# Performance work log

Hardware: AMD Instinct MI355X
Metric: run time of the kernel (lower is better)

Reference implementation:

```python
import jax, jax.numpy as jnp
import numpy as np

NEG = -1e30  # effective -inf that stays stable in fp32 log-sum-exp
BLANK = 0


def _lse3(a, b, c):
    m = jnp.maximum(jnp.maximum(a, b), c)
    return m + jnp.log(jnp.exp(a - m) + jnp.exp(b - m) + jnp.exp(c - m))


def _ctc_loss_sum(log_probs, input_lengths, targets, target_lengths):
    # log_probs: [B, T, V] already log-softmaxed; targets: [B, S] int, blank=0
    B, T, V = log_probs.shape
    S = targets.shape[1]
    L = 2 * S + 1  # extended label seq: blank-interleaved

    ext = jnp.full((B, L), BLANK, dtype=targets.dtype)
    ext = ext.at[:, 1::2].set(targets)  # [B, L]

    # gather per-frame log-probs of extended labels: [B, T, L]
    lp_ext = jnp.take_along_axis(
        log_probs, jnp.broadcast_to(ext[:, None, :], (B, T, L)), axis=2)

    # skip transition s-2 -> s allowed iff ext[s] != blank and ext[s] != ext[s-2]
    ext_prev2 = jnp.pad(ext[:, :-2], ((0, 0), (2, 0)), constant_values=BLANK)
    can_skip = (ext != BLANK) & (ext != ext_prev2) & (jnp.arange(L)[None, :] >= 2)

    # alpha init at t=0
    alpha = jnp.full((B, L), NEG, dtype=log_probs.dtype)
    alpha = alpha.at[:, 0].set(lp_ext[:, 0, 0])
    alpha = alpha.at[:, 1].set(lp_ext[:, 0, 1])

    lp_seq = jnp.swapaxes(lp_ext, 0, 1)[1:]          # [T-1, B, L]
    valid = jnp.arange(1, T)[:, None] < input_lengths[None, :]  # [T-1, B]

    def step(a, xs):
        lp_t, v = xs  # [B, L], [B]
        a1 = jnp.pad(a[:, :-1], ((0, 0), (1, 0)), constant_values=NEG)
        a2 = jnp.pad(a[:, :-2], ((0, 0), (2, 0)), constant_values=NEG)
        a2 = jnp.where(can_skip, a2, NEG)
        new = _lse3(a, a1, a2) + lp_t
        a = jnp.where(v[:, None], new, a)  # freeze past each utterance's length
        return a, None

    alpha, _ = jax.lax.scan(step, alpha, (lp_seq, valid))

    # terminal states: last blank (2*tl) and last label (2*tl - 1)
    end = 2 * target_lengths.astype(jnp.int32)
    aT = jnp.take_along_axis(alpha, jnp.stack([end, end - 1], axis=1), axis=1)  # [B, 2]
    ll = jax.scipy.special.logsumexp(aT, axis=1)
    loss = -ll
    loss = jnp.where(loss > 1e29, 0.0, loss)  # zero_infinity=True
    return jnp.sum(loss)  # reduction='sum'


def setup_inputs() -> dict:
    B, T, V, S = 64, 1024, 512, 128
    key = jax.random.key(0)
    k1, k2, k3, k4 = jax.random.split(key, 4)
    output_tensor = jax.random.normal(k1, (B, T, V), dtype=jnp.float32)
    output_lengths = jax.random.randint(k2, (B,), T // 2, T + 1, dtype=jnp.int32)
    target_tensor = jax.random.randint(k3, (B, S), 1, V, dtype=jnp.int32)  # no blanks
    target_lengths = jax.random.randint(k4, (B,), S // 2, S + 1, dtype=jnp.int32)
    return {"output_tensor": output_tensor, "output_lengths": output_lengths,
            "target_tensor": target_tensor, "target_lengths": target_lengths}


def reference(output_tensor, output_lengths, target_tensor, target_lengths):
    log_probs = jax.nn.log_softmax(output_tensor, axis=2)
    return _ctc_loss_sum(log_probs, output_lengths, target_tensor, target_lengths)
```

## Files before the change

kernel.cpp:

```cpp
#include <hip/hip_runtime.h>
#include <cstdint>

#define T_LEN 1024
#define V_DIM 512
#define S_LEN 128
#define NEG2  (-1.0e30f)
#define PREP_BLOCKS 2048
#define ROWS_PER_WAVE 8

__device__ float2 g_plab[(size_t)64 * T_LEN * 64 + 64];
__device__ float  g_pblank[(size_t)64 * T_LEN + 64];

static __device__ __forceinline__ float dpp_shr1_f(float x) {
    return __int_as_float(__builtin_amdgcn_update_dpp(
        0, __float_as_int(x), 0x138, 0xF, 0xF, true));
}
static __device__ __forceinline__ int dpp_shr1_i(int x) {
    return __builtin_amdgcn_update_dpp(0, x, 0x138, 0xF, 0xF, true);
}
template <int CTRL>
static __device__ __forceinline__ float dpp_add(float x) {
    const int y = __builtin_amdgcn_update_dpp(0, __float_as_int(x), CTRL, 0xF, 0xF, true);
    return x + __int_as_float(y);
}

__global__ __launch_bounds__(256) void ctc_prep(
    const float* __restrict__ x, const int* __restrict__ lens,
    const int* __restrict__ tgts)
{
    const int lane = threadIdx.x & 63;
    const int wv0  = (int)((blockIdx.x * blockDim.x + threadIdx.x) >> 6);
    const float L2E = 1.44269504088896340736f;

    #pragma unroll
    for (int it = 0; it < ROWS_PER_WAVE; ++it) {
        const int wid = wv0 + it * 8192;
        const int b = wid >> 10;
        const int t = wid & (T_LEN - 1);
        if (t >= lens[b]) continue;

        const float* row = x + (size_t)wid * V_DIM;
        const float4 u = *(const float4*)(row + lane * 8);
        const float4 v = *(const float4*)(row + lane * 8 + 4);

        float s = exp2f(u.x * L2E) + exp2f(u.y * L2E)
                + exp2f(u.z * L2E) + exp2f(u.w * L2E)
                + exp2f(v.x * L2E) + exp2f(v.y * L2E)
                + exp2f(v.z * L2E) + exp2f(v.w * L2E);
        s = dpp_add<0x111>(s);
        s = dpp_add<0x112>(s);
        s = dpp_add<0x114>(s);
        s = dpp_add<0x118>(s);
        s = dpp_add<0x142>(s);
        s = dpp_add<0x143>(s);
        const float off =
            log2f(__int_as_float(__builtin_amdgcn_readlane(__float_as_int(s), 63)));

        if (lane == 0) g_pblank[wid] = exp2f(u.x * L2E - off);

        const int2 tg = *(const int2*)(tgts + b * S_LEN + 2 * lane);
        g_plab[(size_t)wid * 64 + lane] =
            make_float2(exp2f(row[tg.x] * L2E - off), exp2f(row[tg.y] * L2E - off));
    }
}

struct AlphaState { float a0, a1, a2, a3, a4; int C; };

static __device__ __forceinline__ void alpha_step(
    AlphaState& st, float pb, float2 lp, float cs1f, float cs3f, bool dead)
{
    const float p3 = dpp_shr1_f(st.a3);
    const int   Cp = dpp_shr1_i(st.C);
    const int   Cn = dead ? Cp : st.C;
    int e = 127 + (Cp - Cn);
    e = e < 0 ? 0 : (e > 252 ? 252 : e);
    const float adj = __int_as_float((unsigned)e << 23);
    const float p3v = p3 * adj;
    const float s01 = st.a0 + st.a1;
    const float s23 = st.a2 + st.a3;
    const float n0 = (st.a0 + p3v) * pb;
    const float n1 = fmaf(p3v, cs1f, s01) * lp.x;
    const float n2 = (st.a1 + st.a2) * pb;
    const float n3 = fmaf(st.a1, cs3f, s23) * lp.y;
    const float n4 = (st.a3 + st.a4) * pb;
    st.a0 = n0; st.a1 = n1; st.a2 = n2; st.a3 = n3; st.a4 = n4; st.C = Cn;
}

static __device__ __forceinline__ void lean_step(
    AlphaState& st, float pb, float2 lp, float cs1f, float cs3f, float adj)
{
    const float p3 = dpp_shr1_f(st.a3);
    const float p3v = p3 * adj;
    const float s01 = st.a0 + st.a1;
    const float s23 = st.a2 + st.a3;
    const float n0 = (st.a0 + p3v) * pb;
    const float n1 = fmaf(p3v, cs1f, s01) * lp.x;
    const float n2 = (st.a1 + st.a2) * pb;
    const float n3 = fmaf(st.a1, cs3f, s23) * lp.y;
    const float n4 = (st.a3 + st.a4) * pb;
    st.a0 = n0; st.a1 = n1; st.a2 = n2; st.a3 = n3; st.a4 = n4;
}

static __device__ __forceinline__ void alpha_rescale(AlphaState& st)
{
    const float mx = fmaxf(fmaxf(fmaxf(st.a0, st.a1), fmaxf(st.a2, st.a3)), st.a4);
    const int ee = (__float_as_int(mx) >> 23) & 255;
    const bool ok = (ee > 0) && (ee < 255);
    const float sc = ok ? __int_as_float((unsigned)(254 - ee) << 23) : 1.0f;
    const int dC = ok ? (ee - 127) : 0;
    st.a0 *= sc; st.a1 *= sc; st.a2 *= sc; st.a3 *= sc; st.a4 *= sc; st.C += dC;
}

struct LGrp  { float2 v[16]; };
struct PBGrp { float4 a, b, c, d; };

static __device__ __forceinline__ float pbsel(const PBGrp& p, int i) {
    const float4 q = (i < 4) ? p.a : (i < 8) ? p.b : (i < 12) ? p.c : p.d;
    const int m = i & 3;
    return m == 0 ? q.x : m == 1 ? q.y : m == 2 ? q.z : q.w;
}

static __device__ __forceinline__ void issueL(
    LGrp& L, const float2* __restrict__ pl_b, int tb, int lenm1, int lane)
{
    #pragma unroll
    for (int j = 0; j < 16; ++j) {
        int r = tb + j; r = (r < lenm1) ? r : lenm1;
        L.v[j] = pl_b[(size_t)r * 64 + lane];
    }
}

static __device__ __forceinline__ void loadPB(PBGrp& P, const float* s) {
    P.a = *(const float4*)(s);
    P.b = *(const float4*)(s + 4);
    P.c = *(const float4*)(s + 8);
    P.d = *(const float4*)(s + 12);
}

template<bool LEAN>
static __device__ __forceinline__ void computeG16(
    AlphaState& st, const LGrp& L, const PBGrp& P,
    float cs1f, float cs3f, int tb, int deadline)
{
    float adj = 1.0f;
    #pragma unroll
    for (int i = 0; i < 16; ++i) {
        if (LEAN) {
            if ((i & 3) == 0) {
                const int Cp = dpp_shr1_i(st.C);
                int e = 127 + (Cp - st.C);
                e = e < 0 ? 0 : (e > 252 ? 252 : e);
                adj = __int_as_float((unsigned)e << 23);
            }
            lean_step(st, pbsel(P, i), L.v[i], cs1f, cs3f, adj);
        } else {
            alpha_step(st, pbsel(P, i), L.v[i], cs1f, cs3f, deadline >= tb + i);
        }
        if ((i & 3) == 3) alpha_rescale(st);
    }
}

static __device__ __forceinline__ void tail_steps(
    AlphaState& st, const LGrp& L, const PBGrp& P,
    float cs1f, float cs3f, int t0, int len, int deadline)
{
    #pragma unroll
    for (int i = 0; i < 15; ++i) {
        if (t0 + i < len) {
            alpha_step(st, pbsel(P, i), L.v[i], cs1f, cs3f, deadline >= t0 + i);
            if ((i & 3) == 3) alpha_rescale(st);
        }
    }
}

#define WAIT16() do { __builtin_amdgcn_sched_barrier(0);  \
    __builtin_amdgcn_s_waitcnt(0x4F70);    \
    __builtin_amdgcn_sched_barrier(0); } while (0)

__global__ __launch_bounds__(64) void ctc_alpha(
    const int* __restrict__ lens, const int* __restrict__ tgts,
    const int* __restrict__ tlens, float* __restrict__ out)
{
    __shared__ alignas(16) float lds_pbs[T_LEN + 16];

    const int b    = blockIdx.x;
    const int lane = threadIdx.x;
    const int len  = lens[b];
    const int tl   = tlens[b];
    const int lenm1 = len - 1;

    const int tA = tgts[b * S_LEN + 2 * lane];
    const int tB = tgts[b * S_LEN + 2 * lane + 1];
    const int tPrev = __shfl_up(tB, 1);
    const bool cs1 = (lane > 0) && (tA != tPrev);
    const bool cs3 = (tB != tA);
    const float cs1f = cs1 ? 1.0f : 0.0f;
    const float cs3f = cs3 ? 1.0f : 0.0f;

    const int repOwn = ((lane > 0 && tA == tPrev) ? 1 : 0) + ((tB == tA) ? 1 : 0);
    int ps = repOwn;
    #pragma unroll
    for (int d = 1; d < 64; d <<= 1) {
        const int y = __shfl_up(ps, d);
        if (lane >= d) ps += y;
    }
    const int deadline = 2 * lane + (ps - repOwn);
    const int dmax = __shfl(deadline, 63);

    const size_t rowb = (size_t)b * T_LEN;
    const float*  __restrict__ pb_b = g_pblank + rowb;
    const float2* __restrict__ pl_b = g_plab + rowb * 64;

    #pragma unroll
    for (int k = 0; k < T_LEN / 64; ++k)
        lds_pbs[k * 64 + lane] = pb_b[k * 64 + lane + 1];

    AlphaState st;
    st.a0 = 0.f; st.a1 = 0.f; st.a2 = 0.f; st.a3 = 0.f; st.a4 = 0.f; st.C = 0;
    if (lane == 0) { st.a0 = pb_b[0]; st.a1 = pl_b[0].x; }

    LGrp LA, LB; PBGrp PA, PB_;
    issueL(LA, pl_b, 1, lenm1, lane);
    loadPB(PA, &lds_pbs[0]);

    int t0 = 1;
    for (; t0 + 32 <= len; t0 += 32) {
        issueL(LB, pl_b, t0 + 16, lenm1, lane);
        loadPB(PB_, &lds_pbs[t0 + 15]);
        WAIT16();
        if (t0 > dmax) computeG16<true >(st, LA, PA, cs1f, cs3f, t0, deadline);
        else           computeG16<false>(st, LA, PA, cs1f, cs3f, t0, deadline);

        issueL(LA, pl_b, t0 + 32, lenm1, lane);
        loadPB(PA, &lds_pbs[t0 + 31]);
        WAIT16();
        if (t0 + 16 > dmax) computeG16<true >(st, LB, PB_, cs1f, cs3f, t0 + 16, deadline);
        else                computeG16<false>(st, LB, PB_, cs1f, cs3f, t0 + 16, deadline);
    }
    if (t0 + 16 <= len) {
        issueL(LB, pl_b, t0 + 16, lenm1, lane);
        loadPB(PB_, &lds_pbs[t0 + 15]);
        WAIT16();
        if (t0 > dmax) computeG16<true >(st, LA, PA, cs1f, cs3f, t0, deadline);
        else           computeG16<false>(st, LA, PA, cs1f, cs3f, t0, deadline);
        t0 += 16;
        __builtin_amdgcn_s_waitcnt(0x0F70);
        __builtin_amdgcn_sched_barrier(0);
        tail_steps(st, LB, PB_, cs1f, cs3f, t0, len, deadline);
    } else {
        __builtin_amdgcn_s_waitcnt(0x0F70);
        __builtin_amdgcn_sched_barrier(0);
        tail_steps(st, LA, PA, cs1f, cs3f, t0, len, deadline);
    }

    const int end = 2 * tl;
    float v1, v2; int C1, C2;
    {
        int s = end;
        int lsrc = s >> 2; if (lsrc > 63) lsrc = 63;
        const int slot = s & 3;
        float cand = (slot == 0) ? st.a0 : (slot == 1) ? st.a1
                   : (slot == 2) ? st.a2 : st.a3;
        if (s == 256) cand = st.a4;
        v1 = __shfl(cand, lsrc);
        C1 = __shfl(st.C, lsrc);

        s = end - 1;
        lsrc = s >> 2;
        const int slot2 = s & 3;
        cand = (slot2 == 0) ? st.a0 : (slot2 == 1) ? st.a1
             : (slot2 == 2) ? st.a2 : st.a3;
        v2 = __shfl(cand, lsrc);
        C2 = __shfl(st.C, lsrc);
    }
    const float l1 = (v1 > 0.f) ? log2f(v1) + (float)C1 : NEG2;
    const float l2 = (v2 > 0.f) ? log2f(v2) + (float)C2 : NEG2;
    const float mM = fmaxf(l1, l2);
    const float ll2 = mM + log2f(exp2f(l1 - mM) + exp2f(l2 - mM));
    float loss = -ll2 * 0.69314718055994530942f;
    if (!(loss < 1e29f)) loss = 0.f;
    if (lane == 0) atomicAdd(out, loss);
}

extern "C" void kernel_launch(void* const* d_in, const int* in_sizes, int n_in,
                              void* d_out, int out_size, void* d_ws, size_t ws_size,
                              hipStream_t stream) {
    (void)in_sizes; (void)n_in; (void)d_ws; (void)ws_size;
    const float* x     = (const float*)d_in[0];
    const int*   lens  = (const int*)d_in[1];
    const int*   tgts  = (const int*)d_in[2];
    const int*   tlens = (const int*)d_in[3];
    float* out = (float*)d_out;

    (void)hipMemsetAsync(d_out, 0, (size_t)out_size * sizeof(float), stream);
    ctc_prep<<<PREP_BLOCKS, 256, 0, stream>>>(x, lens, tgts);
    ctc_alpha<<<64, 64, 0, stream>>>(lens, tgts, tlens, out);
}
```

Before: 258.9 us.

## Pack 16 alpha waves per block, prefetch 8-step groups, readlane blank probs

The alpha recursion kernel now runs 16 utterances per 1024-thread block across 4 blocks, instead of one 64-thread block per utterance. The prefetch granularity drops from 16 to 8 timesteps per double-buffered group, which cuts register pressure. The blank log-prob staging through LDS is replaced: each wave loads 8 values into lanes and broadcasts them with readlane. The intent is to lower per-wave registers and the LDS prologue, but packing waves onto 4 CUs may lower per-wave issue throughput, and the smaller groups expose more load latency.

```diff
diff --git a/kernel.cpp b/kernel.cpp
--- a/kernel.cpp
+++ b/kernel.cpp
@@ -7,6 +7,8 @@
 #define NEG2  (-1.0e30f)
 #define PREP_BLOCKS 2048
 #define ROWS_PER_WAVE 8
+#define WPB   16
+#define ALPHA_BLOCKS 4
 
 __device__ float2 g_plab[(size_t)64 * T_LEN * 64 + 64];
 __device__ float  g_pblank[(size_t)64 * T_LEN + 64];
@@ -111,40 +113,30 @@
     st.a0 *= sc; st.a1 *= sc; st.a2 *= sc; st.a3 *= sc; st.a4 *= sc; st.C += dC;
 }
 
-struct LGrp  { float2 v[16]; };
-struct PBGrp { float4 a, b, c, d; };
-
-static __device__ __forceinline__ float pbsel(const PBGrp& p, int i) {
-    const float4 q = (i < 4) ? p.a : (i < 8) ? p.b : (i < 12) ? p.c : p.d;
-    const int m = i & 3;
-    return m == 0 ? q.x : m == 1 ? q.y : m == 2 ? q.z : q.w;
-}
-
-static __device__ __forceinline__ void issueL(
-    LGrp& L, const float2* __restrict__ pl_b, int tb, int lenm1, int lane)
-{
-    #pragma unroll
-    for (int j = 0; j < 16; ++j) {
+struct LG { float2 v[8]; };
+
+static __device__ __forceinline__ void issue8(
+    LG& L, const float2* __restrict__ pl_b, int tb, int lenm1, int lane)
+{
+    #pragma unroll
+    for (int j = 0; j < 8; ++j) {
         int r = tb + j; r = (r < lenm1) ? r : lenm1;
         L.v[j] = pl_b[(size_t)r * 64 + lane];
     }
 }
 
-static __device__ __forceinline__ void loadPB(PBGrp& P, const float* s) {
-    P.a = *(const float4*)(s);
-    P.b = *(const float4*)(s + 4);
-    P.c = *(const float4*)(s + 8);
-    P.d = *(const float4*)(s + 12);
+static __device__ __forceinline__ float pbr(float pb8, int i) {
+    return __int_as_float(__builtin_amdgcn_readlane(__float_as_int(pb8), i));
 }
 
 template<bool LEAN>
-static __device__ __forceinline__ void computeG16(
-    AlphaState& st, const LGrp& L, const PBGrp& P,
+static __device__ __forceinline__ void compute8(
+    AlphaState& st, const LG& L, float pb8,
     float cs1f, float cs3f, int tb, int deadline)
 {
     float adj = 1.0f;
     #pragma unroll
-    for (int i = 0; i < 16; ++i) {
+    for (int i = 0; i < 8; ++i) {
         if (LEAN) {
             if ((i & 3) == 0) {
                 const int Cp = dpp_shr1_i(st.C);
@@ -152,39 +144,27 @@
                 e = e < 0 ? 0 : (e > 252 ? 252 : e);
                 adj = __int_as_float((unsigned)e << 23);
             }
-            lean_step(st, pbsel(P, i), L.v[i], cs1f, cs3f, adj);
+            lean_step(st, pbr(pb8, i), L.v[i], cs1f, cs3f, adj);
         } else {
-            alpha_step(st, pbsel(P, i), L.v[i], cs1f, cs3f, deadline >= tb + i);
+            alpha_step(st, pbr(pb8, i), L.v[i], cs1f, cs3f, deadline >= tb + i);
         }
         if ((i & 3) == 3) alpha_rescale(st);
     }
 }
 
-static __device__ __forceinline__ void tail_steps(
-    AlphaState& st, const LGrp& L, const PBGrp& P,
-    float cs1f, float cs3f, int t0, int len, int deadline)
-{
-    #pragma unroll
-    for (int i = 0; i < 15; ++i) {
-        if (t0 + i < len) {
-            alpha_step(st, pbsel(P, i), L.v[i], cs1f, cs3f, deadline >= t0 + i);
-            if ((i & 3) == 3) alpha_rescale(st);
-        }
-    }
-}
-
-#define WAIT16() do { __builtin_amdgcn_sched_barrier(0);  \
-    __builtin_amdgcn_s_waitcnt(0x4F70);    \
+#define WAIT9() do { __builtin_amdgcn_sched_barrier(0);  \
+    __builtin_amdgcn_s_waitcnt(0x0F79);    \
     __builtin_amdgcn_sched_barrier(0); } while (0)
-
-__global__ __launch_bounds__(64) void ctc_alpha(
+#define WAIT0() do { __builtin_amdgcn_sched_barrier(0);  \
+    __builtin_amdgcn_s_waitcnt(0x0F70);    \
+    __builtin_amdgcn_sched_barrier(0); } while (0)
+
+__global__ __launch_bounds__(1024) void ctc_alpha(
     const int* __restrict__ lens, const int* __restrict__ tgts,
     const int* __restrict__ tlens, float* __restrict__ out)
 {
-    __shared__ alignas(16) float lds_pbs[T_LEN + 16];
-
-    const int b    = blockIdx.x;
-    const int lane = threadIdx.x;
+    const int lane = threadIdx.x & 63;
+    const int b    = (int)blockIdx.x * WPB + (int)(threadIdx.x >> 6);
     const int len  = lens[b];
     const int tl   = tlens[b];
     const int lenm1 = len - 1;
@@ -211,46 +191,47 @@
     const float*  __restrict__ pb_b = g_pblank + rowb;
     const float2* __restrict__ pl_b = g_plab + rowb * 64;
 
-    #pragma unroll
-    for (int k = 0; k < T_LEN / 64; ++k)
-        lds_pbs[k * 64 + lane] = pb_b[k * 64 + lane + 1];
-
     AlphaState st;
     st.a0 = 0.f; st.a1 = 0.f; st.a2 = 0.f; st.a3 = 0.f; st.a4 = 0.f; st.C = 0;
     if (lane == 0) { st.a0 = pb_b[0]; st.a1 = pl_b[0].x; }
 
-    LGrp LA, LB; PBGrp PA, PB_;
-    issueL(LA, pl_b, 1, lenm1, lane);
-    loadPB(PA, &lds_pbs[0]);
+    LG LA, LB; float pbA, pbB;
+    issue8(LA, pl_b, 1, lenm1, lane);
+    pbA = pb_b[1 + (lane & 7)];
 
     int t0 = 1;
-    for (; t0 + 32 <= len; t0 += 32) {
-        issueL(LB, pl_b, t0 + 16, lenm1, lane);
-        loadPB(PB_, &lds_pbs[t0 + 15]);
-        WAIT16();
-        if (t0 > dmax) computeG16<true >(st, LA, PA, cs1f, cs3f, t0, deadline);
-        else           computeG16<false>(st, LA, PA, cs1f, cs3f, t0, deadline);
-
-        issueL(LA, pl_b, t0 + 32, lenm1, lane);
-        loadPB(PA, &lds_pbs[t0 + 31]);
-        WAIT16();
-        if (t0 + 16 > dmax) computeG16<true >(st, LB, PB_, cs1f, cs3f, t0 + 16, deadline);
-        else                computeG16<false>(st, LB, PB_, cs1f, cs3f, t0 + 16, deadline);
-    }
-    if (t0 + 16 <= len) {
-        issueL(LB, pl_b, t0 + 16, lenm1, lane);
-        loadPB(PB_, &lds_pbs[t0 + 15]);
-        WAIT16();
-        if (t0 > dmax) computeG16<true >(st, LA, PA, cs1f, cs3f, t0, deadline);
-        else           computeG16<false>(st, LA, PA, cs1f, cs3f, t0, deadline);
-        t0 += 16;
-        __builtin_amdgcn_s_waitcnt(0x0F70);
-        __builtin_amdgcn_sched_barrier(0);
-        tail_steps(st, LB, PB_, cs1f, cs3f, t0, len, deadline);
-    } else {
-        __builtin_amdgcn_s_waitcnt(0x0F70);
-        __builtin_amdgcn_sched_barrier(0);
-        tail_steps(st, LA, PA, cs1f, cs3f, t0, len, deadline);
+    for (; t0 + 16 <= len; t0 += 16) {
+        issue8(LB, pl_b, t0 + 8, lenm1, lane);
+        pbB = pb_b[t0 + 8 + (lane & 7)];
+        WAIT9();
+        if (t0 > dmax) compute8<true >(st, LA, pbA, cs1f, cs3f, t0, deadline);
+        else           compute8<false>(st, LA, pbA, cs1f, cs3f, t0, deadline);
+
+        issue8(LA, pl_b, t0 + 16, lenm1, lane);
+        pbA = pb_b[t0 + 16 + (lane & 7)];
+        WAIT9();
+        if (t0 + 8 > dmax) compute8<true >(st, LB, pbB, cs1f, cs3f, t0 + 8, deadline);
+        else               compute8<false>(st, LB, pbB, cs1f, cs3f, t0 + 8, deadline);
+    }
+    if (t0 + 8 < len) {
+        issue8(LB, pl_b, t0 + 8, lenm1, lane);
+        pbB = pb_b[t0 + 8 + (lane & 7)];
+    }
+    WAIT0();
+    #pragma unroll
+    for (int i = 0; i < 8; ++i) {
+        if (t0 + i < len) {
+            alpha_step(st, pbr(pbA, i), LA.v[i], cs1f, cs3f, deadline >= t0 + i);
+            if ((i & 3) == 3) alpha_rescale(st);
+        }
+    }
+    #pragma unroll
+    for (int i = 8; i < 16; ++i) {
+        if (t0 + i < len) {
+            alpha_step(st, pbr(pbB, i - 8), LB.v[i - 8], cs1f, cs3f,
+                       deadline >= t0 + i);
+            if ((i & 3) == 3) alpha_rescale(st);
+        }
     }
 
     const int end = 2 * tl;
@@ -294,5 +275,5 @@
 
     (void)hipMemsetAsync(d_out, 0, (size_t)out_size * sizeof(float), stream);
     ctc_prep<<<PREP_BLOCKS, 256, 0, stream>>>(x, lens, tgts);
-    ctc_alpha<<<64, 64, 0, stream>>>(lens, tgts, tlens, out);
-}
+    ctc_alpha<<<ALPHA_BLOCKS, WPB * 64, 0, stream>>>(lens, tgts, tlens, out);
+}
```

New measurement: 351.6 us. 1.36x slower.
